# Kernel tuning notes

Measured on AMD Instinct MI355X. Metric: run time of the kernel, lower is better.

Reference implementation:

```python
import jax, jax.numpy as jnp
import numpy as np

HID = 128
OUT = 128
NC = 100000
NA = 1024
FC = 256
FA = 4096

def _sage(x_src, x_dst, ei, Wl, bl, Wr):
    # PyG SAGEConv, mean aggregation, bipartite:
    # out[i] = lin_l(mean_{j->i} x_src[j]) + lin_r(x_dst[i])
    n_dst = x_dst.shape[0]
    src, dst = ei[0], ei[1]
    msg = x_src[src]                                  # [E, F_src] gather
    agg = jax.ops.segment_sum(msg, dst, num_segments=n_dst)
    cnt = jax.ops.segment_sum(jnp.ones((ei.shape[1],), x_src.dtype), dst, num_segments=n_dst)
    mean = agg / jnp.clip(cnt, 1.0, None)[:, None]
    return mean @ Wl.T + bl + x_dst @ Wr.T

def setup_inputs() -> dict:
    key = jax.random.key(0)
    ks = jax.random.split(key, 20)
    d = {}
    d["article_x"] = jax.random.normal(ks[0], (1, FA), jnp.float32)
    d["community_x"] = jax.random.normal(ks[1], (NC, FC), jnp.float32)
    # bipartite edges: row = article node idx (<NA), col = community idx (<NC)
    d["e_wb"] = jnp.stack([jax.random.randint(ks[2], (500000,), 0, NA, jnp.int32),
                            jax.random.randint(ks[3], (500000,), 0, NC, jnp.int32)])
    d["e_mb"] = jnp.stack([jax.random.randint(ks[4], (500000,), 0, NA, jnp.int32),
                            jax.random.randint(ks[5], (500000,), 0, NC, jnp.int32)])
    d["e_cc"] = jax.random.randint(ks[6], (2, 800000), 0, NC, jnp.int32)
    s = lambda k, sh: jax.random.normal(k, sh, jnp.float32) * (1.0 / np.sqrt(sh[-1]))
    d["W_lin1"] = s(ks[7], (NA, FA)); d["b_lin1"] = jnp.zeros((NA,), jnp.float32)
    d["Wl1"] = s(ks[8], (HID, 1));   d["bl1"] = jnp.zeros((HID,), jnp.float32); d["Wr1"] = s(ks[9], (HID, FC))
    d["Wl2"] = s(ks[10], (HID, 1));  d["bl2"] = jnp.zeros((HID,), jnp.float32); d["Wr2"] = s(ks[11], (HID, HID))
    d["Wl3"] = s(ks[12], (HID, HID)); d["bl3"] = jnp.zeros((HID,), jnp.float32); d["Wr3"] = s(ks[13], (HID, FC))
    d["W_lin2"] = s(ks[14], (OUT, HID)); d["b_lin2"] = jnp.zeros((OUT,), jnp.float32)
    d["Wd1"] = s(ks[15], (OUT, 2 * OUT)); d["bd1"] = jnp.zeros((OUT,), jnp.float32)
    d["Wd2"] = s(ks[16], (1, OUT)); d["bd2"] = jnp.zeros((1,), jnp.float32)
    return d

def reference(article_x, community_x, e_wb, e_mb, e_cc,
              W_lin1, b_lin1, Wl1, bl1, Wr1, Wl2, bl2, Wr2,
              Wl3, bl3, Wr3, W_lin2, b_lin2, Wd1, bd1, Wd2, bd2):
    # encoder
    art = (article_x @ W_lin1.T + b_lin1).reshape(NA, 1)      # [1024, 1]
    h1 = jax.nn.relu(_sage(art, community_x, e_wb, Wl1, bl1, Wr1))   # [NC, HID]
    h2 = jax.nn.relu(_sage(art, h1, e_mb, Wl2, bl2, Wr2))            # [NC, HID]
    h3 = jax.nn.relu(_sage(h2, community_x, e_cc, Wl3, bl3, Wr3))    # [NC, HID]
    z = h3 @ W_lin2.T + b_lin2                                       # [NC, OUT]
    # edge decoder on interacts_with edges
    row, col = e_cc[0], e_cc[1]
    zz = jnp.concatenate([z[row], z[col]], axis=-1)                  # [E, 2*OUT]
    h = jax.nn.relu(zz @ Wd1.T + bd1)
    return (h @ Wd2.T + bd2).reshape(-1)                             # [E]
```

## Files before the change

kernel.cpp:

```cpp
#include <hip/hip_runtime.h>

#define NC 100000
#define NA 1024
#define FA 4096
#define MAXD 40

typedef _Float16 half8 __attribute__((ext_vector_type(8)));
typedef _Float16 half4v __attribute__((ext_vector_type(4)));
typedef _Float16 half2v __attribute__((ext_vector_type(2)));
typedef float floatx4 __attribute__((ext_vector_type(4)));

#define CNT_OFF 4294967296.0
#define CNT_INV 2.3283064365386963e-10

__device__ __forceinline__ void cvt_range(const float* __restrict__ in,
                                          _Float16* __restrict__ out, int n4,
                                          int bid, int nb) {
    int t = bid * 256 + threadIdx.x;
    int stride = nb * 256;
    for (int i = t; i < n4; i += stride) {
        float4 v = ((const float4*)in)[i];
        half4v h = {(_Float16)v.x, (_Float16)v.y, (_Float16)v.z, (_Float16)v.w};
        ((half4v*)out)[i] = h;
    }
}

__device__ __forceinline__ void edge_seg(const int* __restrict__ ei, int E,
                                         const float* __restrict__ art,
                                         double* __restrict__ acd, int bid, int nb) {
    int t = bid * 256 + threadIdx.x;
    int stride = nb * 256;
    for (int e = t; e < E; e += stride) {
        int s = ei[e], d = ei[E + e];
        atomicAdd(&acd[d], (double)art[s] + CNT_OFF);
    }
}

__device__ __forceinline__ void scat_seg(const int* __restrict__ ei, int E,
                                         int* __restrict__ cnt, int2* __restrict__ se2,
                                         int bid, int nb) {
    int t = bid * 256 + threadIdx.x;
    int stride = nb * 256;
    for (int e = t; e < E; e += stride) {
        int s = ei[e], d = ei[E + e];
        int pos = atomicAdd(&cnt[d], 1);
        if (pos < MAXD) se2[(size_t)d * MAXD + pos] = make_int2(s, e);
    }
}

__device__ __forceinline__ void wcomb_seg(const float* __restrict__ Wd1,
                                          const float* __restrict__ Wlin2,
                                          _Float16* __restrict__ Wuh,
                                          _Float16* __restrict__ Wvh, int bid) {
    int i = bid * 2 + (threadIdx.x >> 7);
    int j = threadIdx.x & 127;
    float au = 0.f, av = 0.f;
    for (int m = 0; m < 128; ++m) {
        float wl = Wlin2[m * 128 + j];
        au = fmaf(Wd1[i * 256 + m], wl, au);
        av = fmaf(Wd1[i * 256 + 128 + m], wl, av);
    }
    Wuh[i * 128 + j] = (_Float16)au;
    Wvh[i * 128 + j] = (_Float16)av;
}

__device__ __forceinline__ void bcomb_seg(const float* __restrict__ Wd1,
                                          const float* __restrict__ b2,
                                          const float* __restrict__ bd1,
                                          float* __restrict__ bu, float* __restrict__ bv) {
    int i = threadIdx.x;
    if (i >= 128) return;
    float su = 0.f, sv = 0.f;
    for (int m = 0; m < 128; ++m) {
        float b = b2[m];
        su = fmaf(Wd1[i * 256 + m], b, su);
        sv = fmaf(Wd1[i * 256 + 128 + m], b, sv);
    }
    bu[i] = su + bd1[i];
    bv[i] = sv;
}

#define ART_BLKS 256
#define Z1_BLKS  64
#define Z2_BLKS  16
__global__ void k_art(const float* __restrict__ ax, const float* __restrict__ W,
                      const float* __restrict__ b, float* __restrict__ art,
                      float4* __restrict__ zacd, float4* __restrict__ zcnt) {
    int blk = blockIdx.x;
    if (blk >= ART_BLKS) {
        blk -= ART_BLKS;
        float4 z = make_float4(0.f, 0.f, 0.f, 0.f);
        if (blk < Z1_BLKS) {
            int n4 = 2 * NC * 2 / 4;
            int t = blk * 256 + threadIdx.x;
            for (int i = t; i < n4; i += Z1_BLKS * 256) zacd[i] = z;
        } else {
            blk -= Z1_BLKS;
            int n4 = NC / 4;
            int t = blk * 256 + threadIdx.x;
            for (int i = t; i < n4; i += Z2_BLKS * 256) zcnt[i] = z;
        }
        return;
    }
    int wave = (blk * 256 + threadIdx.x) >> 6;
    int lane = threadIdx.x & 63;
    if (wave >= NA) return;
    const float* wr = W + (size_t)wave * FA;
    float s = 0.f;
    #pragma unroll
    for (int i = 0; i < FA; i += 256) {
        float4 a  = *(const float4*)&ax[i + 4 * lane];
        float4 wv = *(const float4*)&wr[i + 4 * lane];
        s += a.x * wv.x + a.y * wv.y + a.z * wv.z + a.w * wv.w;
    }
    for (int off = 32; off; off >>= 1) s += __shfl_down(s, off);
    if (lane == 0) art[wave] = s + b[wave];
}

#define FRONT_WB   1024
#define FRONT_MB   1024
#define FRONT_SC   768
#define FRONT_WCVT 96
#define FRONT_WCOMB 64
#define FRONT_BCOMB 1
#define FRONT_CVT  8192
#define FRONT_TOTAL (FRONT_WB + FRONT_MB + FRONT_SC + FRONT_WCVT + FRONT_WCOMB + FRONT_BCOMB + FRONT_CVT)

__global__ __launch_bounds__(256)
void k_front(const int* __restrict__ e_wb, int E1,
             const int* __restrict__ e_mb, int E2,
             const int* __restrict__ e_cc, int E3,
             const float* __restrict__ art,
             double* __restrict__ acd1, double* __restrict__ acd2,
             int* __restrict__ cnt3, int2* __restrict__ se2,
             const float* __restrict__ Wr1, _Float16* __restrict__ Wr1h,
             const float* __restrict__ Wr2, _Float16* __restrict__ Wr2h,
             const float* __restrict__ Wl3, _Float16* __restrict__ Wl3h,
             const float* __restrict__ Wr3, _Float16* __restrict__ Wr3h,
             const float* __restrict__ Wd1, const float* __restrict__ Wlin2,
             _Float16* __restrict__ Wuh, _Float16* __restrict__ Wvh,
             const float* __restrict__ b2, const float* __restrict__ bd1,
             float* __restrict__ bu, float* __restrict__ bv,
             const float* __restrict__ cx, _Float16* __restrict__ cxh)
{
    int b = blockIdx.x;
    if (b < FRONT_WB) { edge_seg(e_wb, E1, art, acd1, b, FRONT_WB); return; }
    b -= FRONT_WB;
    if (b < FRONT_MB) { edge_seg(e_mb, E2, art, acd2, b, FRONT_MB); return; }
    b -= FRONT_MB;
    if (b < FRONT_SC) { scat_seg(e_cc, E3, cnt3, se2, b, FRONT_SC); return; }
    b -= FRONT_SC;
    if (b < FRONT_WCVT) {
        if (b < 32) cvt_range(Wr1, Wr1h, 8192, b, 32);
        else if (b < 48) cvt_range(Wr2, Wr2h, 4096, b - 32, 16);
        else if (b < 64) cvt_range(Wl3, Wl3h, 4096, b - 48, 16);
        else cvt_range(Wr3, Wr3h, 8192, b - 64, 32);
        return;
    }
    b -= FRONT_WCVT;
    if (b < FRONT_WCOMB) { wcomb_seg(Wd1, Wlin2, Wuh, Wvh, b); return; }
    b -= FRONT_WCOMB;
    if (b < FRONT_BCOMB) { bcomb_seg(Wd1, b2, bd1, bu, bv); return; }
    b -= FRONT_BCOMB;
    cvt_range(cx, cxh, NC * 64, b, FRONT_CVT);
}

__device__ __forceinline__ float mean_from_packed(double t) {
    double cd = rint(t * CNT_INV);
    float sum = (float)(t - cd * CNT_OFF);
    float cc = (float)cd;
    cc = cc > 1.f ? cc : 1.f;
    return sum / cc;
}

#define MID_GB  ((NC + 127) / 128)

__global__ __launch_bounds__(256)
void k_enc12(const _Float16* __restrict__ cxh, const _Float16* __restrict__ Wr1h,
             const _Float16* __restrict__ Wr2h,
             const float* __restrict__ bl1, const double* __restrict__ acd1,
             const float* __restrict__ Wl1,
             const float* __restrict__ bl2, const double* __restrict__ acd2,
             const float* __restrict__ Wl2,
             _Float16* __restrict__ out, int N)
{
    __shared__ _Float16 lds[128 * 40 + 128 * 136];
    _Float16* Bh  = lds;
    _Float16* Ah  = lds + 128 * 40;
    _Float16* h1t = lds + 128 * 40;

    const int t = threadIdx.x, lane = t & 63, w = t >> 6;
    const int rowbase = blockIdx.x * 128;
    const bool isA = t < 128;
    const int rr = isA ? t : t - 128;
    const int fr = lane & 15;
    const int kq = (lane >> 4) << 3;

    floatx4 zero4 = {0.f, 0.f, 0.f, 0.f};
    floatx4 acc[2][8];
    #pragma unroll
    for (int i = 0; i < 2; ++i)
        #pragma unroll
        for (int cf = 0; cf < 8; ++cf) acc[i][cf] = zero4;

    float4 p0, p1, p2, p3;
    float4 zf = make_float4(0.f, 0.f, 0.f, 0.f);
    {
        bool ok = true; const _Float16* base;
        if (isA) { int row = rowbase + rr; ok = row < N; base = ok ? &cxh[(size_t)row * 256] : Ah; }
        else base = &Wr1h[(size_t)rr * 256];
        const float4* s4 = (const float4*)base;
        p0 = ok ? s4[0] : zf; p1 = ok ? s4[1] : zf; p2 = ok ? s4[2] : zf; p3 = ok ? s4[3] : zf;
    }
    for (int tile = 0; tile < 8; ++tile) {
        float4* dst = (float4*)(isA ? &Ah[rr * 40] : &Bh[rr * 40]);
        dst[0] = p0; dst[1] = p1; dst[2] = p2; dst[3] = p3;
        __syncthreads();
        if (tile < 7) {
            int ko = (tile + 1) << 5;
            bool ok = true; const _Float16* base;
            if (isA) { int row = rowbase + rr; ok = row < N; base = ok ? &cxh[(size_t)row * 256 + ko] : Ah; }
            else base = &Wr1h[(size_t)rr * 256 + ko];
            const float4* s4 = (const float4*)base;
            p0 = ok ? s4[0] : zf; p1 = ok ? s4[1] : zf; p2 = ok ? s4[2] : zf; p3 = ok ? s4[3] : zf;
        }
        half8 af0 = *(const half8*)&Ah[(w * 32 + fr) * 40 + kq];
        half8 af1 = *(const half8*)&Ah[(w * 32 + 16 + fr) * 40 + kq];
        #pragma unroll
        for (int cf = 0; cf < 8; ++cf) {
            half8 bf = *(const half8*)&Bh[(cf * 16 + fr) * 40 + kq];
            acc[0][cf] = __builtin_amdgcn_mfma_f32_16x16x32_f16(af0, bf, acc[0][cf], 0, 0, 0);
            acc[1][cf] = __builtin_amdgcn_mfma_f32_16x16x32_f16(af1, bf, acc[1][cf], 0, 0, 0);
        }
        __syncthreads();
    }

    {
        float blc[8], wlc[8];
        #pragma unroll
        for (int cf = 0; cf < 8; ++cf) { int col = cf * 16 + fr; blc[cf] = bl1[col]; wlc[cf] = Wl1[col]; }
        #pragma unroll
        for (int i = 0; i < 2; ++i) {
            #pragma unroll
            for (int j = 0; j < 4; ++j) {
                int lrow = w * 32 + i * 16 + ((lane >> 4) << 2) + j;
                int grow = rowbase + lrow;
                float m = 0.f;
                if (grow < N) m = mean_from_packed(acd1[grow]);
                #pragma unroll
                for (int cf = 0; cf < 8; ++cf) {
                    float v = acc[i][cf][j] + blc[cf] + m * wlc[cf];
                    v = fmaxf(v, 0.f);
                    h1t[lrow * 136 + cf * 16 + fr] = (_Float16)v;
                }
            }
        }
    }
    __syncthreads();

    #pragma unroll
    for (int i = 0; i < 2; ++i)
        #pragma unroll
        for (int cf = 0; cf < 8; ++cf) acc[i][cf] = zero4;
    if (!isA) {
        const float4* s4 = (const float4*)&Wr2h[(size_t)rr * 128];
        p0 = s4[0]; p1 = s4[1]; p2 = s4[2]; p3 = s4[3];
    }
    for (int tt = 0; tt < 4; ++tt) {
        if (!isA) { float4* d = (float4*)&Bh[rr * 40]; d[0] = p0; d[1] = p1; d[2] = p2; d[3] = p3; }
        __syncthreads();
        if (!isA && tt < 3) {
            const float4* s4 = (const float4*)&Wr2h[(size_t)rr * 128 + ((tt + 1) << 5)];
            p0 = s4[0]; p1 = s4[1]; p2 = s4[2]; p3 = s4[3];
        }
        half8 af0 = *(const half8*)&h1t[(w * 32 + fr) * 136 + (tt << 5) + kq];
        half8 af1 = *(const half8*)&h1t[(w * 32 + 16 + fr) * 136 + (tt << 5) + kq];
        #pragma unroll
        for (int cf = 0; cf < 8; ++cf) {
            half8 bf = *(const half8*)&Bh[(cf * 16 + fr) * 40 + kq];
            acc[0][cf] = __builtin_amdgcn_mfma_f32_16x16x32_f16(af0, bf, acc[0][cf], 0, 0, 0);
            acc[1][cf] = __builtin_amdgcn_mfma_f32_16x16x32_f16(af1, bf, acc[1][cf], 0, 0, 0);
        }
        __syncthreads();
    }

    {
        float blc[8], wlc[8];
        #pragma unroll
        for (int cf = 0; cf < 8; ++cf) { int col = cf * 16 + fr; blc[cf] = bl2[col]; wlc[cf] = Wl2[col]; }
        #pragma unroll
        for (int i = 0; i < 2; ++i) {
            #pragma unroll
            for (int j = 0; j < 4; ++j) {
                int grow = rowbase + w * 32 + i * 16 + ((lane >> 4) << 2) + j;
                if (grow < N) {
                    float m = mean_from_packed(acd2[grow]);
                    #pragma unroll
                    for (int cf = 0; cf < 8; ++cf) {
                        float v = acc[i][cf][j] + blc[cf] + m * wlc[cf];
                        v = fmaxf(v, 0.f);
                        out[(size_t)grow * 128 + cf * 16 + fr] = (_Float16)v;
                    }
                }
            }
        }
    }
}

__global__ __launch_bounds__(256)
void k_csr_agg_h(const int* __restrict__ cnt3, const int2* __restrict__ se2,
                 const _Float16* __restrict__ h, _Float16* __restrict__ agg) {
    int node = (blockIdx.x * blockDim.x + threadIdx.x) >> 6;
    int lane = threadIdx.x & 63;
    if (node >= NC) return;
    int d = cnt3[node]; if (d > MAXD) d = MAXD;
    const int2* bucket = se2 + (size_t)node * MAXD;
    int sj = 0;
    if (lane < d) sj = bucket[lane].x;
    float sx = 0.f, sy = 0.f;
    #pragma unroll 4
    for (int j = 0; j < d; ++j) {
        int src = __shfl(sj, j);
        half2v m = *(const half2v*)&h[(size_t)src * 128 + 2 * lane];
        sx += (float)m[0]; sy += (float)m[1];
    }
    half2v r = {(_Float16)sx, (_Float16)sy};
    *(half2v*)&agg[(size_t)node * 128 + 2 * lane] = r;
}

__global__ __launch_bounds__(256)
void k_enc3uv(const _Float16* __restrict__ aggh, const _Float16* __restrict__ Wl3h,
              const _Float16* __restrict__ cxh, const _Float16* __restrict__ Wr3h,
              const float* __restrict__ bl3, const int* __restrict__ rcnt,
              const _Float16* __restrict__ Wuh, const float* __restrict__ bu,
              const _Float16* __restrict__ Wvh, const float* __restrict__ bv,
              _Float16* __restrict__ uout, _Float16* __restrict__ vout, int N)
{
    __shared__ _Float16 lds[128 * 40 + 128 * 136];
    _Float16* Bh  = lds;
    _Float16* Ah  = lds + 128 * 40;
    _Float16* h3t = lds + 128 * 40;

    const int t = threadIdx.x, lane = t & 63, w = t >> 6;
    const int rowbase = blockIdx.x * 128;
    const bool isA = t < 128;
    const int rr = isA ? t : t - 128;
    const int fr = lane & 15;
    const int kq = (lane >> 4) << 3;

    floatx4 zero4 = {0.f, 0.f, 0.f, 0.f};
    floatx4 acc[2][8];
    #pragma unroll
    for (int i = 0; i < 2; ++i)
        #pragma unroll
        for (int cf = 0; cf < 8; ++cf) acc[i][cf] = zero4;

    float4 p0, p1, p2, p3;
    float4 zf = make_float4(0.f, 0.f, 0.f, 0.f);
    {
        bool ok = true; const _Float16* base;
        if (isA) { int row = rowbase + rr; ok = row < N; base = ok ? &aggh[(size_t)row * 128] : Ah; }
        else base = &Wl3h[(size_t)rr * 128];
        const float4* s4 = (const float4*)base;
        p0 = ok ? s4[0] : zf; p1 = ok ? s4[1] : zf; p2 = ok ? s4[2] : zf; p3 = ok ? s4[3] : zf;
    }
    for (int tile = 0; tile < 12; ++tile) {
        float4* dst = (float4*)(isA ? &Ah[rr * 40] : &Bh[rr * 40]);
        dst[0] = p0; dst[1] = p1; dst[2] = p2; dst[3] = p3;
        __syncthreads();
        if (tile < 11) {
            int tn = tile + 1;
            bool ok = true; const _Float16* base;
            if (tn < 4) {
                int ko = tn << 5;
                if (isA) { int row = rowbase + rr; ok = row < N; base = ok ? &aggh[(size_t)row * 128 + ko] : Ah; }
                else base = &Wl3h[(size_t)rr * 128 + ko];
            } else {
                int ko = (tn - 4) << 5;
                if (isA) { int row = rowbase + rr; ok = row < N; base = ok ? &cxh[(size_t)row * 256 + ko] : Ah; }
                else base = &Wr3h[(size_t)rr * 256 + ko];
            }
            const float4* s4 = (const float4*)base;
            p0 = ok ? s4[0] : zf; p1 = ok ? s4[1] : zf; p2 = ok ? s4[2] : zf; p3 = ok ? s4[3] : zf;
        }
        half8 af0 = *(const half8*)&Ah[(w * 32 + fr) * 40 + kq];
        half8 af1 = *(const half8*)&Ah[(w * 32 + 16 + fr) * 40 + kq];
        #pragma unroll
        for (int cf = 0; cf < 8; ++cf) {
            half8 bf = *(const half8*)&Bh[(cf * 16 + fr) * 40 + kq];
            acc[0][cf] = __builtin_amdgcn_mfma_f32_16x16x32_f16(af0, bf, acc[0][cf], 0, 0, 0);
            acc[1][cf] = __builtin_amdgcn_mfma_f32_16x16x32_f16(af1, bf, acc[1][cf], 0, 0, 0);
        }
        if (tile == 3) {
            #pragma unroll
            for (int i = 0; i < 2; ++i)
                #pragma unroll
                for (int j = 0; j < 4; ++j) {
                    int row = rowbase + w * 32 + i * 16 + ((lane >> 4) << 2) + j;
                    float c = (row < N) ? (float)rcnt[row] : 1.f;
                    c = c > 1.f ? c : 1.f;
                    float inv = 1.f / c;
                    #pragma unroll
                    for (int cf = 0; cf < 8; ++cf) acc[i][cf][j] *= inv;
                }
        }
        __syncthreads();
    }

    {
        float blc[8];
        #pragma unroll
        for (int cf = 0; cf < 8; ++cf) blc[cf] = bl3[cf * 16 + fr];
        #pragma unroll
        for (int i = 0; i < 2; ++i) {
            #pragma unroll
            for (int j = 0; j < 4; ++j) {
                int lrow = w * 32 + i * 16 + ((lane >> 4) << 2) + j;
                #pragma unroll
                for (int cf = 0; cf < 8; ++cf) {
                    float v = acc[i][cf][j] + blc[cf];
                    v = fmaxf(v, 0.f);
                    h3t[lrow * 136 + cf * 16 + fr] = (_Float16)v;
                }
            }
        }
    }
    __syncthreads();

    for (int ph = 0; ph < 2; ++ph) {
        const _Float16* Wp = ph ? Wvh : Wuh;
        const float* bp = ph ? bv : bu;
        _Float16* op = ph ? vout : uout;
        #pragma unroll
        for (int i = 0; i < 2; ++i)
            #pragma unroll
            for (int cf = 0; cf < 8; ++cf) acc[i][cf] = zero4;
        if (!isA) {
            const float4* s4 = (const float4*)&Wp[(size_t)rr * 128];
            p0 = s4[0]; p1 = s4[1]; p2 = s4[2]; p3 = s4[3];
        }
        for (int tt = 0; tt < 4; ++tt) {
            if (!isA) { float4* d = (float4*)&Bh[rr * 40]; d[0] = p0; d[1] = p1; d[2] = p2; d[3] = p3; }
            __syncthreads();
            if (!isA && tt < 3) {
                const float4* s4 = (const float4*)&Wp[(size_t)rr * 128 + ((tt + 1) << 5)];
                p0 = s4[0]; p1 = s4[1]; p2 = s4[2]; p3 = s4[3];
            }
            half8 af0 = *(const half8*)&h3t[(w * 32 + fr) * 136 + (tt << 5) + kq];
            half8 af1 = *(const half8*)&h3t[(w * 32 + 16 + fr) * 136 + (tt << 5) + kq];
            #pragma unroll
            for (int cf = 0; cf < 8; ++cf) {
                half8 bf = *(const half8*)&Bh[(cf * 16 + fr) * 40 + kq];
                acc[0][cf] = __builtin_amdgcn_mfma_f32_16x16x32_f16(af0, bf, acc[0][cf], 0, 0, 0);
                acc[1][cf] = __builtin_amdgcn_mfma_f32_16x16x32_f16(af1, bf, acc[1][cf], 0, 0, 0);
            }
            __syncthreads();
        }
        float bc[8];
        #pragma unroll
        for (int cf = 0; cf < 8; ++cf) bc[cf] = bp[cf * 16 + fr];
        #pragma unroll
        for (int i = 0; i < 2; ++i) {
            #pragma unroll
            for (int j = 0; j < 4; ++j) {
                int grow = rowbase + w * 32 + i * 16 + ((lane >> 4) << 2) + j;
                if (grow < N) {
                    #pragma unroll
                    for (int cf = 0; cf < 8; ++cf)
                        op[(size_t)grow * 128 + cf * 16 + fr] = (_Float16)(acc[i][cf][j] + bc[cf]);
                }
            }
        }
    }
}

__global__ __launch_bounds__(256)
void k_decoder_h(const int* __restrict__ cnt3, const int2* __restrict__ se2,
                 const _Float16* __restrict__ u, const _Float16* __restrict__ v,
                 const float* __restrict__ wd2, const float* __restrict__ bd2,
                 float* __restrict__ out) {
    int node = (blockIdx.x * blockDim.x + threadIdx.x) >> 6;
    if (node >= NC) return;
    int lane = threadIdx.x & 63;
    int g = lane >> 3, s = lane & 7;

    float wf[16], vf[16];
    #pragma unroll
    for (int q = 0; q < 16; ++q) wf[q] = wd2[s * 16 + q];
    {
        half8 va = *(const half8*)&v[(size_t)node * 128 + s * 16];
        half8 vb = *(const half8*)&v[(size_t)node * 128 + s * 16 + 8];
        #pragma unroll
        for (int q = 0; q < 8; ++q) { vf[q] = (float)va[q]; vf[8 + q] = (float)vb[q]; }
    }
    float bb = bd2[0];

    int d = cnt3[node]; if (d > MAXD) d = MAXD;
    const int2* bucket = se2 + (size_t)node * MAXD;
    int sj = 0, ej = 0;
    if (lane < d) { int2 p = bucket[lane]; sj = p.x; ej = p.y; }

    for (int jb = 0; jb < d; jb += 8) {
        int j = jb + g;
        float p = 0.f;
        bool act = j < d;
        int src = __shfl(sj, j);
        int eid = __shfl(ej, j);
        if (act) {
            half8 ua = *(const half8*)&u[(size_t)src * 128 + s * 16];
            half8 ub = *(const half8*)&u[(size_t)src * 128 + s * 16 + 8];
            #pragma unroll
            for (int q = 0; q < 8; ++q) {
                p = fmaf(wf[q],     fmaxf((float)ua[q] + vf[q],     0.f), p);
                p = fmaf(wf[8 + q], fmaxf((float)ub[q] + vf[8 + q], 0.f), p);
            }
        }
        p += __shfl_xor(p, 1);
        p += __shfl_xor(p, 2);
        p += __shfl_xor(p, 4);
        if (act && s == 0) out[eid] = p + bb;
    }
}

extern "C" void kernel_launch(void* const* d_in, const int* in_sizes, int n_in,
                              void* d_out, int out_size, void* d_ws, size_t ws_size,
                              hipStream_t stream) {
    const float* article_x = (const float*)d_in[0];
    const float* cx     = (const float*)d_in[1];
    const int*   e_wb   = (const int*)d_in[2];
    const int*   e_mb   = (const int*)d_in[3];
    const int*   e_cc   = (const int*)d_in[4];
    const float* W_lin1 = (const float*)d_in[5];
    const float* b_lin1 = (const float*)d_in[6];
    const float* Wl1    = (const float*)d_in[7];
    const float* bl1    = (const float*)d_in[8];
    const float* Wr1    = (const float*)d_in[9];
    const float* Wl2    = (const float*)d_in[10];
    const float* bl2    = (const float*)d_in[11];
    const float* Wr2    = (const float*)d_in[12];
    const float* Wl3    = (const float*)d_in[13];
    const float* bl3    = (const float*)d_in[14];
    const float* Wr3    = (const float*)d_in[15];
    const float* W_lin2 = (const float*)d_in[16];
    const float* b_lin2 = (const float*)d_in[17];
    const float* Wd1    = (const float*)d_in[18];
    const float* bd1    = (const float*)d_in[19];
    const float* Wd2    = (const float*)d_in[20];
    const float* bd2    = (const float*)d_in[21];
    float* out = (float*)d_out;

    const int E1 = in_sizes[2] / 2;
    const int E2 = in_sizes[3] / 2;
    const int E3 = in_sizes[4] / 2;

    double* acd1 = (double*)d_ws;
    double* acd2 = acd1 + NC;
    float* ws = (float*)(acd2 + NC);
    size_t o = 0;
    float* art   = ws;      o += 1024;
    float* buf   = ws + o;  o += 128;
    float* bvf   = ws + o;  o += 128;
    int* cnt3   = (int*)(ws + o); o += NC;
    int2* se2   = (int2*)(ws + o); o += (size_t)2 * NC * MAXD;
    _Float16* hws = (_Float16*)(ws + o);
    size_t ho = 0;
    _Float16* cxh    = hws + ho; ho += (size_t)NC * 256;
    _Float16* B1h    = hws + ho; ho += (size_t)NC * 128;
    _Float16* B2h    = hws + ho; ho += (size_t)NC * 128;
    _Float16* Wr1h   = hws + ho; ho += 128 * 256;
    _Float16* Wr2h   = hws + ho; ho += 128 * 128;
    _Float16* Wl3h   = hws + ho; ho += 128 * 128;
    _Float16* Wr3h   = hws + ho; ho += 128 * 256;
    _Float16* Wuh    = hws + ho; ho += 128 * 128;
    _Float16* Wvh    = hws + ho; ho += 128 * 128;

    k_art<<<ART_BLKS + Z1_BLKS + Z2_BLKS, 256, 0, stream>>>(
        article_x, W_lin1, b_lin1, art, (float4*)acd1, (float4*)cnt3);

    k_front<<<FRONT_TOTAL, 256, 0, stream>>>(
        e_wb, E1, e_mb, E2, e_cc, E3, art, acd1, acd2, cnt3, se2,
        Wr1, Wr1h, Wr2, Wr2h, Wl3, Wl3h, Wr3, Wr3h,
        Wd1, W_lin2, Wuh, Wvh, b_lin2, bd1, buf, bvf, cx, cxh);

    k_enc12<<<MID_GB, 256, 0, stream>>>(
        cxh, Wr1h, Wr2h, bl1, acd1, Wl1, bl2, acd2, Wl2, B1h, NC);

    const int GW = (NC * 64 + 255) / 256;
    k_csr_agg_h<<<GW, 256, 0, stream>>>(cnt3, se2, B1h, B2h);
    k_enc3uv<<<MID_GB, 256, 0, stream>>>(B2h, Wl3h, cxh, Wr3h,
                                         bl3, cnt3, Wuh, buf, Wvh, bvf,
                                         B1h, B2h, NC);
    k_decoder_h<<<GW, 256, 0, stream>>>(cnt3, se2, B1h, B2h, Wd2, bd2, out);
}
```

Before: 317.7 us.

## Move first SAGE GEMM into front kernel to overlap with edge scatter

The cx@Wr1 MFMA GEMM moves out of the encoder kernel and into the multi-role front kernel as extra blocks. These blocks read fp32 community features and weights directly and convert them to fp16 in LDS. They spill raw accumulators to a new fp32 workspace buffer, which the renamed encoder kernel reloads before applying the epilogue and the second GEMM. The goal is to overlap GEMM compute with the atomic-heavy edge-aggregation segments and drop the Wr1 conversion. The cost is a large extra accumulator write and read, plus LDS now being allocated for every front block, which may lower occupancy for the other segments.

```diff
diff --git a/kernel.cpp b/kernel.cpp
--- a/kernel.cpp
+++ b/kernel.cpp
@@ -80,6 +80,120 @@
     bv[i] = sv;
 }
 
+__device__ __forceinline__ void enc12_p1(_Float16* lds, int blk,
+                                         const float* __restrict__ cx,
+                                         const float* __restrict__ Wr1,
+                                         floatx4* __restrict__ accbuf, int N)
+{
+    _Float16* Ah = lds;
+    _Float16* Bh = lds + 128 * 40;
+    const int t = threadIdx.x, lane = t & 63, w = t >> 6;
+    const int rowbase = blk * 128;
+    const bool isA = t < 128;
+    const int rr = isA ? t : t - 128;
+    const int fr = lane & 15;
+    const int kq = (lane >> 4) << 3;
+
+    floatx4 zero4 = {0.f, 0.f, 0.f, 0.f};
+    floatx4 acc[2][8];
+    #pragma unroll
+    for (int i = 0; i < 2; ++i)
+        #pragma unroll
+        for (int cf = 0; cf < 8; ++cf) acc[i][cf] = zero4;
+
+    float4 pf[8];
+    float4 zf = make_float4(0.f, 0.f, 0.f, 0.f);
+    const float* srcrow = isA ? &cx[(size_t)(rowbase + rr) * 256] : &Wr1[(size_t)rr * 256];
+    bool ok = !isA || (rowbase + rr) < N;
+    {
+        const float4* s4 = (const float4*)(ok ? srcrow : cx);
+        #pragma unroll
+        for (int i = 0; i < 8; ++i) pf[i] = ok ? s4[i] : zf;
+    }
+    for (int tile = 0; tile < 8; ++tile) {
+        half4v* d = (half4v*)(isA ? &Ah[rr * 40] : &Bh[rr * 40]);
+        #pragma unroll
+        for (int i = 0; i < 8; ++i) {
+            float4 v = pf[i];
+            half4v h = {(_Float16)v.x, (_Float16)v.y, (_Float16)v.z, (_Float16)v.w};
+            d[i] = h;
+        }
+        __syncthreads();
+        if (tile < 7) {
+            const float4* s4 = (const float4*)(ok ? srcrow + ((tile + 1) << 5) : cx);
+            #pragma unroll
+            for (int i = 0; i < 8; ++i) pf[i] = ok ? s4[i] : zf;
+        }
+        half8 af0 = *(const half8*)&Ah[(w * 32 + fr) * 40 + kq];
+        half8 af1 = *(const half8*)&Ah[(w * 32 + 16 + fr) * 40 + kq];
+        #pragma unroll
+        for (int cf = 0; cf < 8; ++cf) {
+            half8 bf = *(const half8*)&Bh[(cf * 16 + fr) * 40 + kq];
+            acc[0][cf] = __builtin_amdgcn_mfma_f32_16x16x32_f16(af0, bf, acc[0][cf], 0, 0, 0);
+            acc[1][cf] = __builtin_amdgcn_mfma_f32_16x16x32_f16(af1, bf, acc[1][cf], 0, 0, 0);
+        }
+        __syncthreads();
+    }
+    floatx4* ob = accbuf + ((size_t)(blk * 4 + w) * 16) * 64 + lane;
+    #pragma unroll
+    for (int i = 0; i < 2; ++i)
+        #pragma unroll
+        for (int cf = 0; cf < 8; ++cf)
+            ob[(size_t)(i * 8 + cf) * 64] = acc[i][cf];
+}
+
+#define FRONT_P1   782
+#define FRONT_WB   1024
+#define FRONT_MB   1024
+#define FRONT_SC   768
+#define FRONT_WCVT 96
+#define FRONT_WCOMB 64
+#define FRONT_BCOMB 1
+#define FRONT_CVT  8192
+#define FRONT_TOTAL (FRONT_P1 + FRONT_WB + FRONT_MB + FRONT_SC + FRONT_WCVT + FRONT_WCOMB + FRONT_BCOMB + FRONT_CVT)
+
+__global__ __launch_bounds__(256)
+void k_front(const int* __restrict__ e_wb, int E1,
+             const int* __restrict__ e_mb, int E2,
+             const int* __restrict__ e_cc, int E3,
+             const float* __restrict__ art,
+             double* __restrict__ acd1, double* __restrict__ acd2,
+             int* __restrict__ cnt3, int2* __restrict__ se2,
+             const float* __restrict__ cxf, const float* __restrict__ Wr1f,
+             floatx4* __restrict__ accbuf,
+             const float* __restrict__ Wr2, _Float16* __restrict__ Wr2h,
+             const float* __restrict__ Wl3, _Float16* __restrict__ Wl3h,
+             const float* __restrict__ Wr3, _Float16* __restrict__ Wr3h,
+             const float* __restrict__ Wd1, const float* __restrict__ Wlin2,
+             _Float16* __restrict__ Wuh, _Float16* __restrict__ Wvh,
+             const float* __restrict__ b2, const float* __restrict__ bd1,
+             float* __restrict__ bu, float* __restrict__ bv,
+             _Float16* __restrict__ cxh)
+{
+    __shared__ _Float16 lds[2 * 128 * 40];
+    int b = blockIdx.x;
+    if (b < FRONT_P1) { enc12_p1(lds, b, cxf, Wr1f, accbuf, NC); return; }
+    b -= FRONT_P1;
+    if (b < FRONT_WB) { edge_seg(e_wb, E1, art, acd1, b, FRONT_WB); return; }
+    b -= FRONT_WB;
+    if (b < FRONT_MB) { edge_seg(e_mb, E2, art, acd2, b, FRONT_MB); return; }
+    b -= FRONT_MB;
+    if (b < FRONT_SC) { scat_seg(e_cc, E3, cnt3, se2, b, FRONT_SC); return; }
+    b -= FRONT_SC;
+    if (b < FRONT_WCVT) {
+        if (b < 16) cvt_range(Wr2, Wr2h, 4096, b, 16);
+        else if (b < 32) cvt_range(Wl3, Wl3h, 4096, b - 16, 16);
+        else cvt_range(Wr3, Wr3h, 8192, b - 32, 64);
+        return;
+    }
+    b -= FRONT_WCVT;
+    if (b < FRONT_WCOMB) { wcomb_seg(Wd1, Wlin2, Wuh, Wvh, b); return; }
+    b -= FRONT_WCOMB;
+    if (b < FRONT_BCOMB) { bcomb_seg(Wd1, b2, bd1, bu, bv); return; }
+    b -= FRONT_BCOMB;
+    cvt_range(cxf, cxh, NC * 64, b, FRONT_CVT);
+}
+
 #define ART_BLKS 256
 #define Z1_BLKS  64
 #define Z2_BLKS  16
@@ -91,7 +205,7 @@
         blk -= ART_BLKS;
         float4 z = make_float4(0.f, 0.f, 0.f, 0.f);
         if (blk < Z1_BLKS) {
-            int n4 = 2 * NC * 2 / 4;
+            int n4 = NC;
             int t = blk * 256 + threadIdx.x;
             for (int i = t; i < n4; i += Z1_BLKS * 256) zacd[i] = z;
         } else {
@@ -117,54 +231,6 @@
     if (lane == 0) art[wave] = s + b[wave];
 }
 
-#define FRONT_WB   1024
-#define FRONT_MB   1024
-#define FRONT_SC   768
-#define FRONT_WCVT 96
-#define FRONT_WCOMB 64
-#define FRONT_BCOMB 1
-#define FRONT_CVT  8192
-#define FRONT_TOTAL (FRONT_WB + FRONT_MB + FRONT_SC + FRONT_WCVT + FRONT_WCOMB + FRONT_BCOMB + FRONT_CVT)
-
-__global__ __launch_bounds__(256)
-void k_front(const int* __restrict__ e_wb, int E1,
-             const int* __restrict__ e_mb, int E2,
-             const int* __restrict__ e_cc, int E3,
-             const float* __restrict__ art,
-             double* __restrict__ acd1, double* __restrict__ acd2,
-             int* __restrict__ cnt3, int2* __restrict__ se2,
-             const float* __restrict__ Wr1, _Float16* __restrict__ Wr1h,
-             const float* __restrict__ Wr2, _Float16* __restrict__ Wr2h,
-             const float* __restrict__ Wl3, _Float16* __restrict__ Wl3h,
-             const float* __restrict__ Wr3, _Float16* __restrict__ Wr3h,
-             const float* __restrict__ Wd1, const float* __restrict__ Wlin2,
-             _Float16* __restrict__ Wuh, _Float16* __restrict__ Wvh,
-             const float* __restrict__ b2, const float* __restrict__ bd1,
-             float* __restrict__ bu, float* __restrict__ bv,
-             const float* __restrict__ cx, _Float16* __restrict__ cxh)
-{
-    int b = blockIdx.x;
-    if (b < FRONT_WB) { edge_seg(e_wb, E1, art, acd1, b, FRONT_WB); return; }
-    b -= FRONT_WB;
-    if (b < FRONT_MB) { edge_seg(e_mb, E2, art, acd2, b, FRONT_MB); return; }
-    b -= FRONT_MB;
-    if (b < FRONT_SC) { scat_seg(e_cc, E3, cnt3, se2, b, FRONT_SC); return; }
-    b -= FRONT_SC;
-    if (b < FRONT_WCVT) {
-        if (b < 32) cvt_range(Wr1, Wr1h, 8192, b, 32);
-        else if (b < 48) cvt_range(Wr2, Wr2h, 4096, b - 32, 16);
-        else if (b < 64) cvt_range(Wl3, Wl3h, 4096, b - 48, 16);
-        else cvt_range(Wr3, Wr3h, 8192, b - 64, 32);
-        return;
-    }
-    b -= FRONT_WCVT;
-    if (b < FRONT_WCOMB) { wcomb_seg(Wd1, Wlin2, Wuh, Wvh, b); return; }
-    b -= FRONT_WCOMB;
-    if (b < FRONT_BCOMB) { bcomb_seg(Wd1, b2, bd1, bu, bv); return; }
-    b -= FRONT_BCOMB;
-    cvt_range(cx, cxh, NC * 64, b, FRONT_CVT);
-}
-
 __device__ __forceinline__ float mean_from_packed(double t) {
     double cd = rint(t * CNT_INV);
     float sum = (float)(t - cd * CNT_OFF);
@@ -176,17 +242,15 @@
 #define MID_GB  ((NC + 127) / 128)
 
 __global__ __launch_bounds__(256)
-void k_enc12(const _Float16* __restrict__ cxh, const _Float16* __restrict__ Wr1h,
-             const _Float16* __restrict__ Wr2h,
-             const float* __restrict__ bl1, const double* __restrict__ acd1,
-             const float* __restrict__ Wl1,
-             const float* __restrict__ bl2, const double* __restrict__ acd2,
-             const float* __restrict__ Wl2,
-             _Float16* __restrict__ out, int N)
+void k_enc12b(const floatx4* __restrict__ accbuf, const _Float16* __restrict__ Wr2h,
+              const float* __restrict__ bl1, const double* __restrict__ acd1,
+              const float* __restrict__ Wl1,
+              const float* __restrict__ bl2, const double* __restrict__ acd2,
+              const float* __restrict__ Wl2,
+              _Float16* __restrict__ out, int N)
 {
     __shared__ _Float16 lds[128 * 40 + 128 * 136];
     _Float16* Bh  = lds;
-    _Float16* Ah  = lds + 128 * 40;
     _Float16* h1t = lds + 128 * 40;
 
     const int t = threadIdx.x, lane = t & 63, w = t >> 6;
@@ -198,41 +262,13 @@
 
     floatx4 zero4 = {0.f, 0.f, 0.f, 0.f};
     floatx4 acc[2][8];
-    #pragma unroll
-    for (int i = 0; i < 2; ++i)
-        #pragma unroll
-        for (int cf = 0; cf < 8; ++cf) acc[i][cf] = zero4;
-
-    float4 p0, p1, p2, p3;
-    float4 zf = make_float4(0.f, 0.f, 0.f, 0.f);
     {
-        bool ok = true; const _Float16* base;
-        if (isA) { int row = rowbase + rr; ok = row < N; base = ok ? &cxh[(size_t)row * 256] : Ah; }
-        else base = &Wr1h[(size_t)rr * 256];
-        const float4* s4 = (const float4*)base;
-        p0 = ok ? s4[0] : zf; p1 = ok ? s4[1] : zf; p2 = ok ? s4[2] : zf; p3 = ok ? s4[3] : zf;
-    }
-    for (int tile = 0; tile < 8; ++tile) {
-        float4* dst = (float4*)(isA ? &Ah[rr * 40] : &Bh[rr * 40]);
-        dst[0] = p0; dst[1] = p1; dst[2] = p2; dst[3] = p3;
-        __syncthreads();
-        if (tile < 7) {
-            int ko = (tile + 1) << 5;
-            bool ok = true; const _Float16* base;
-            if (isA) { int row = rowbase + rr; ok = row < N; base = ok ? &cxh[(size_t)row * 256 + ko] : Ah; }
-            else base = &Wr1h[(size_t)rr * 256 + ko];
-            const float4* s4 = (const float4*)base;
-            p0 = ok ? s4[0] : zf; p1 = ok ? s4[1] : zf; p2 = ok ? s4[2] : zf; p3 = ok ? s4[3] : zf;
-        }
-        half8 af0 = *(const half8*)&Ah[(w * 32 + fr) * 40 + kq];
-        half8 af1 = *(const half8*)&Ah[(w * 32 + 16 + fr) * 40 + kq];
-        #pragma unroll
-        for (int cf = 0; cf < 8; ++cf) {
-            half8 bf = *(const half8*)&Bh[(cf * 16 + fr) * 40 + kq];
-            acc[0][cf] = __builtin_amdgcn_mfma_f32_16x16x32_f16(af0, bf, acc[0][cf], 0, 0, 0);
-            acc[1][cf] = __builtin_amdgcn_mfma_f32_16x16x32_f16(af1, bf, acc[1][cf], 0, 0, 0);
-        }
-        __syncthreads();
+        const floatx4* ib = accbuf + ((size_t)(blockIdx.x * 4 + w) * 16) * 64 + lane;
+        #pragma unroll
+        for (int i = 0; i < 2; ++i)
+            #pragma unroll
+            for (int cf = 0; cf < 8; ++cf)
+                acc[i][cf] = ib[(size_t)(i * 8 + cf) * 64];
     }
 
     {
@@ -262,6 +298,7 @@
     for (int i = 0; i < 2; ++i)
         #pragma unroll
         for (int cf = 0; cf < 8; ++cf) acc[i][cf] = zero4;
+    float4 p0, p1, p2, p3;
     if (!isA) {
         const float4* s4 = (const float4*)&Wr2h[(size_t)rr * 128];
         p0 = s4[0]; p1 = s4[1]; p2 = s4[2]; p3 = s4[3];
@@ -560,6 +597,8 @@
     float* art   = ws;      o += 1024;
     float* buf   = ws + o;  o += 128;
     float* bvf   = ws + o;  o += 128;
+    o = (o + 3) & ~(size_t)3;
+    floatx4* accbuf = (floatx4*)(ws + o); o += (size_t)MID_GB * 4 * 16 * 64 * 4;
     int* cnt3   = (int*)(ws + o); o += NC;
     int2* se2   = (int2*)(ws + o); o += (size_t)2 * NC * MAXD;
     _Float16* hws = (_Float16*)(ws + o);
@@ -567,7 +606,6 @@
     _Float16* cxh    = hws + ho; ho += (size_t)NC * 256;
     _Float16* B1h    = hws + ho; ho += (size_t)NC * 128;
     _Float16* B2h    = hws + ho; ho += (size_t)NC * 128;
-    _Float16* Wr1h   = hws + ho; ho += 128 * 256;
     _Float16* Wr2h   = hws + ho; ho += 128 * 128;
     _Float16* Wl3h   = hws + ho; ho += 128 * 128;
     _Float16* Wr3h   = hws + ho; ho += 128 * 256;
@@ -579,11 +617,12 @@
 
     k_front<<<FRONT_TOTAL, 256, 0, stream>>>(
         e_wb, E1, e_mb, E2, e_cc, E3, art, acd1, acd2, cnt3, se2,
-        Wr1, Wr1h, Wr2, Wr2h, Wl3, Wl3h, Wr3, Wr3h,
-        Wd1, W_lin2, Wuh, Wvh, b_lin2, bd1, buf, bvf, cx, cxh);
-
-    k_enc12<<<MID_GB, 256, 0, stream>>>(
-        cxh, Wr1h, Wr2h, bl1, acd1, Wl1, bl2, acd2, Wl2, B1h, NC);
+        cx, Wr1, accbuf,
+        Wr2, Wr2h, Wl3, Wl3h, Wr3, Wr3h,
+        Wd1, W_lin2, Wuh, Wvh, b_lin2, bd1, buf, bvf, cxh);
+
+    k_enc12b<<<MID_GB, 256, 0, stream>>>(
+        accbuf, Wr2h, bl1, acd1, Wl1, bl2, acd2, Wl2, B1h, NC);
 
     const int GW = (NC * 64 + 255) / 256;
     k_csr_agg_h<<<GW, 256, 0, stream>>>(cnt3, se2, B1h, B2h);
```

Result: slower. 490.2 us (+54.3%).
